# Kernel tuning notes

Hardware: AMD Instinct MI355X
Metric: run time of the kernel (lower is better)

The kernel has to match this reference:

```python
import jax, jax.numpy as jnp
import numpy as np

TEMPERATURE = 0.01  # clamped min is 0.01, so constant temp stays 0.01
MASK_VAL = -10000.0


def setup_inputs() -> dict:
    key = jax.random.key(0)
    k1, k2 = jax.random.split(key)
    B, C, D = 512, 16, 128
    ts_features = jax.random.normal(k1, (B, C, D), dtype=jnp.float32)
    note_features = jax.random.normal(k2, (B, C, D), dtype=jnp.float32)
    return {"ts_features": ts_features, "note_features": note_features}


def reference(ts_features, note_features):
    B, C, D = ts_features.shape
    N = B * C
    ts = ts_features.reshape(N, D)
    nt = note_features.reshape(N, D)

    # sim[i, j] = <ts_i, nt_j>
    sim = jnp.einsum('id,jd->ij', ts, nt)

    # block-diagonal mask: within each CxC block, off-diagonal -> -10000, diagonal kept
    idx = jnp.arange(N)
    blk = idx // C
    same_block = blk[:, None] == blk[None, :]
    is_diag = idx[:, None] == idx[None, :]
    sim_new = jnp.where(same_block & ~is_diag, jnp.asarray(MASK_VAL, sim.dtype), sim)

    logits = sim_new / TEMPERATURE
    # cross entropy with labels = arange(N), both directions
    lsm_r = jax.nn.log_softmax(logits, axis=-1)
    lsm_c = jax.nn.log_softmax(logits.T, axis=-1)
    diag_ids = (idx, idx)
    ce_r = -jnp.mean(lsm_r[diag_ids])
    ce_c = -jnp.mean(lsm_c[diag_ids])
    total_loss = (ce_r + ce_c) / 2

    # nan/inf -> 0 as in the original
    total_loss = jnp.where(jnp.isnan(total_loss) | jnp.isinf(total_loss),
                           jnp.asarray(0.0, total_loss.dtype), total_loss)
    return total_loss
```

## Files before the change

### kernel.cpp

```cpp
#include <hip/hip_runtime.h>
#include <stdint.h>

#define NROWS 8192
#define DDIM  128
#define PPART 8
#define BROWS 256
#define NITER 16
#define LOG2E_X100 144.26950408889634f
#define LN2F       0.6931471805599453f

typedef __bf16 bf16x8 __attribute__((ext_vector_type(8)));
typedef float  f32x4  __attribute__((ext_vector_type(4)));

__device__ __forceinline__ unsigned short f2bf_rne(float f) {
    union { float f; uint32_t u; } v; v.f = f;
    uint32_t r = (v.u + 0x7FFFu + ((v.u >> 16) & 1u)) >> 16;
    return (unsigned short)r;
}

__device__ __forceinline__ void async16(const unsigned short* g, unsigned char* l) {
    __builtin_amdgcn_global_load_lds(
        (const __attribute__((address_space(1))) unsigned int*)g,
        (__attribute__((address_space(3))) unsigned int*)l, 16, 0, 0);
}

__global__ void convert_kernel(const float* __restrict__ ts, const float* __restrict__ nt,
                               unsigned short* __restrict__ ts_bf,
                               unsigned short* __restrict__ nt_bf,
                               float* __restrict__ acc, int* __restrict__ ticket) {
    const int nvec = (NROWS * DDIM) / 4;
    int tid = blockIdx.x * blockDim.x + threadIdx.x;
    bool isNT = tid >= nvec;
    int i = isNT ? (tid - nvec) : tid;
    const float4 v = ((const float4*)(isNT ? nt : ts))[i];
    float sc = isNT ? 1.0f : LOG2E_X100;
    ushort4 o;
    o.x = f2bf_rne(v.x * sc); o.y = f2bf_rne(v.y * sc);
    o.z = f2bf_rne(v.z * sc); o.w = f2bf_rne(v.w * sc);
    ((ushort4*)(isNT ? nt_bf : ts_bf))[i] = o;
    if (tid == 0) { *acc = 0.0f; *ticket = 0; }
}

__device__ __forceinline__ void dma_stage(const unsigned short* g, unsigned char* l,
                                          int lane, int wv) {
#pragma unroll
    for (int k = 0; k < 2; ++k) {
        int u = wv * 2 + k;
        int r = u * 4 + (lane >> 4);
        int ch = (lane & 15) ^ (r & 7);
        async16(g + r * 128 + ch * 8, l + u * 1024);
    }
}

__global__ __launch_bounds__(512, 4) void rowstats_kernel(
        const unsigned short* __restrict__ ts_bf,
        const unsigned short* __restrict__ nt_bf,
        float* __restrict__ pm, float* __restrict__ ps, float* __restrict__ pd) {
    __shared__ unsigned char smem[2 * 16384];

    const int lane = threadIdx.x & 63;
    const int wv   = threadIdx.x >> 6;
    const int c    = lane & 15;
    const int quad = lane >> 4;
    const int bx   = blockIdx.x;
    const int part = blockIdx.y;
    const int dir  = blockIdx.z;
    const int rows0 = bx * BROWS + wv * 32;

    const unsigned short* A = dir ? nt_bf : ts_bf;
    const unsigned short* B = dir ? ts_bf : nt_bf;

    bf16x8 a[2][4];
#pragma unroll
    for (int s = 0; s < 2; ++s) {
        const unsigned short* abase = A + (rows0 + s * 16 + c) * DDIM + quad * 8;
#pragma unroll
        for (int kc = 0; kc < 4; ++kc)
            a[s][kc] = *(const bf16x8*)(abase + kc * 32);
    }

    float m[2][4], ss[2][4], dg[2][4];
#pragma unroll
    for (int s = 0; s < 2; ++s)
#pragma unroll
        for (int r = 0; r < 4; ++r) { m[s][r] = -INFINITY; ss[s][r] = 0.0f; dg[s][r] = 0.0f; }

    const bool havePart = (part == (bx >> 2));
    const int  t_d = (bx & 3) * 4 + (wv >> 1);
    const int  l0  = (wv & 1) * 2;

    const unsigned short* bwalk = B + part * (NROWS / PPART) * DDIM;

    dma_stage(bwalk, smem, lane, wv);
    __syncthreads();

    for (int t = 0; t < NITER; ++t) {
        if (t + 1 < NITER)
            dma_stage(bwalk + (t + 1) * 64 * DDIM, smem + ((t + 1) & 1) * 16384, lane, wv);

        const unsigned char* buf = smem + (t & 1) * 16384;

        f32x4 acc[4][2];
#pragma unroll
        for (int l = 0; l < 4; ++l)
#pragma unroll
            for (int s = 0; s < 2; ++s) acc[l][s] = (f32x4){0.f, 0.f, 0.f, 0.f};

#pragma unroll
        for (int kc = 0; kc < 4; ++kc) {
            const int sw = ((kc * 4 + quad) ^ (c & 7)) * 16;
            const unsigned char* p = buf + c * 256 + sw;
            bf16x8 b0 = *(const bf16x8*)(p);
            bf16x8 b1 = *(const bf16x8*)(p + 4096);
            bf16x8 b2 = *(const bf16x8*)(p + 8192);
            bf16x8 b3 = *(const bf16x8*)(p + 12288);
            acc[0][0] = __builtin_amdgcn_mfma_f32_16x16x32_bf16(a[0][kc], b0, acc[0][0], 0, 0, 0);
            acc[0][1] = __builtin_amdgcn_mfma_f32_16x16x32_bf16(a[1][kc], b0, acc[0][1], 0, 0, 0);
            acc[1][0] = __builtin_amdgcn_mfma_f32_16x16x32_bf16(a[0][kc], b1, acc[1][0], 0, 0, 0);
            acc[1][1] = __builtin_amdgcn_mfma_f32_16x16x32_bf16(a[1][kc], b1, acc[1][1], 0, 0, 0);
            acc[2][0] = __builtin_amdgcn_mfma_f32_16x16x32_bf16(a[0][kc], b2, acc[2][0], 0, 0, 0);
            acc[2][1] = __builtin_amdgcn_mfma_f32_16x16x32_bf16(a[1][kc], b2, acc[2][1], 0, 0, 0);
            acc[3][0] = __builtin_amdgcn_mfma_f32_16x16x32_bf16(a[0][kc], b3, acc[3][0], 0, 0, 0);
            acc[3][1] = __builtin_amdgcn_mfma_f32_16x16x32_bf16(a[1][kc], b3, acc[3][1], 0, 0, 0);
        }

        const bool pd_ = havePart && (t == t_d);
#pragma unroll
        for (int s = 0; s < 2; ++s) {
#pragma unroll
            for (int r = 0; r < 4; ++r) {
                float x0 = acc[0][s][r], x1 = acc[1][s][r];
                float x2 = acc[2][s][r], x3 = acc[3][s][r];
                if (pd_) {
                    const int dslot = l0 + s;
                    bool onDiag = (c == quad * 4 + r);
                    float xv = dslot == 0 ? x0 : dslot == 1 ? x1 : dslot == 2 ? x2 : x3;
                    if (onDiag) dg[s][r] += xv;
                    float rep = onDiag ? xv : -1.0e30f;
                    if (dslot == 0) x0 = rep; else if (dslot == 1) x1 = rep;
                    else if (dslot == 2) x2 = rep; else x3 = rep;
                }
                float mn = fmaxf(fmaxf(fmaxf(x0, x1), fmaxf(x2, x3)), m[s][r]);
                float e  = __builtin_amdgcn_exp2f(m[s][r] - mn);
                float es = (__builtin_amdgcn_exp2f(x0 - mn) + __builtin_amdgcn_exp2f(x1 - mn))
                         + (__builtin_amdgcn_exp2f(x2 - mn) + __builtin_amdgcn_exp2f(x3 - mn));
                ss[s][r] = fmaf(ss[s][r], e, es);
                m[s][r] = mn;
            }
        }
        __syncthreads();
    }

#pragma unroll
    for (int s = 0; s < 2; ++s) {
#pragma unroll
        for (int r = 0; r < 4; ++r) {
            float mm = m[s][r];
#pragma unroll
            for (int off = 1; off < 16; off <<= 1)
                mm = fmaxf(mm, __shfl_xor(mm, off, 64));
            float sv = ss[s][r] * __builtin_amdgcn_exp2f(m[s][r] - mm);
            float dd = dg[s][r];
#pragma unroll
            for (int off = 1; off < 16; off <<= 1) {
                sv += __shfl_xor(sv, off, 64);
                dd += __shfl_xor(dd, off, 64);
            }
            if (c == 0) {
                int row = rows0 + s * 16 + quad * 4 + r;
                int idx = (dir * NROWS + row) * PPART + part;
                pm[idx] = mm; ps[idx] = sv; pd[idx] = dd;
            }
        }
    }
}

__global__ void merge_kernel(const float* __restrict__ pm, const float* __restrict__ ps,
                             const float* __restrict__ pd, float* __restrict__ acc,
                             int* __restrict__ ticket, float* __restrict__ out) {
    int tid = blockIdx.x * blockDim.x + threadIdx.x;
    const float* pmr = pm + tid * PPART;
    const float* psr = ps + tid * PPART;
    const float* pdr = pd + tid * PPART;
    float mt = -INFINITY;
#pragma unroll
    for (int p = 0; p < PPART; ++p) mt = fmaxf(mt, pmr[p]);
    float st = 0.0f, dt = 0.0f;
#pragma unroll
    for (int p = 0; p < PPART; ++p) {
        st += psr[p] * __builtin_amdgcn_exp2f(pmr[p] - mt);
        dt += pdr[p];
    }
    float lsm = dt - mt - __builtin_amdgcn_logf(st);

    float v = lsm;
#pragma unroll
    for (int off = 32; off; off >>= 1) v += __shfl_down(v, off, 64);
    __shared__ float wsum[4];
    if ((threadIdx.x & 63) == 0) wsum[threadIdx.x >> 6] = v;
    __syncthreads();
    if (threadIdx.x == 0) {
        atomicAdd(acc, wsum[0] + wsum[1] + wsum[2] + wsum[3]);
        __threadfence();
        int old = atomicAdd(ticket, 1);
        if (old == (int)gridDim.x - 1) {
            __threadfence();
            float tot = atomicAdd(acc, 0.0f);
            float t = -(tot * LN2F) / (2.0f * NROWS);
            if (!isfinite(t)) t = 0.0f;
            out[0] = t;
        }
    }
}

extern "C" void kernel_launch(void* const* d_in, const int* in_sizes, int n_in,
                              void* d_out, int out_size, void* d_ws, size_t ws_size,
                              hipStream_t stream) {
    const float* ts = (const float*)d_in[0];
    const float* nt = (const float*)d_in[1];
    float* out = (float*)d_out;

    unsigned short* ts_bf = (unsigned short*)d_ws;
    unsigned short* nt_bf = ts_bf + NROWS * DDIM;
    float* pm = (float*)(nt_bf + NROWS * DDIM);
    float* ps = pm + 2 * NROWS * PPART;
    float* pd = ps + 2 * NROWS * PPART;
    float* acc = pd + 2 * NROWS * PPART;
    int* ticket = (int*)(acc + 1);

    convert_kernel<<<2048, 256, 0, stream>>>(ts, nt, ts_bf, nt_bf, acc, ticket);
    rowstats_kernel<<<dim3(NROWS / BROWS, PPART, 2), 512, 0, stream>>>(ts_bf, nt_bf, pm, ps, pd);
    merge_kernel<<<(2 * NROWS) / 256, 256, 0, stream>>>(pm, ps, pd, acc, ticket, out);
}
```

Baseline: 110.0 us.

## Drop LDS staging for direct B loads and fuse merge into rowstats kernel

The rowstats kernel no longer stages B tiles into LDS with async global_load_lds double buffering. Each wave now loads B fragments straight from global memory into registers, which removes the per-iteration __syncthreads. The separate merge kernel is folded into rowstats: per-(dir, block-row) counters pick the last of the partition blocks to finish, and that block merges the partial stats and adds its sum to the global accumulator. This removes one kernel launch and the extra pass over the partials. In exchange, B reuse across the 8 waves now depends on the L1/L2 caches, and there is extra atomic and fence traffic at the end of each block.

```diff
diff --git a/kernel.cpp b/kernel.cpp
--- a/kernel.cpp
+++ b/kernel.cpp
@@ -18,16 +18,10 @@
     return (unsigned short)r;
 }
 
-__device__ __forceinline__ void async16(const unsigned short* g, unsigned char* l) {
-    __builtin_amdgcn_global_load_lds(
-        (const __attribute__((address_space(1))) unsigned int*)g,
-        (__attribute__((address_space(3))) unsigned int*)l, 16, 0, 0);
-}
-
 __global__ void convert_kernel(const float* __restrict__ ts, const float* __restrict__ nt,
                                unsigned short* __restrict__ ts_bf,
                                unsigned short* __restrict__ nt_bf,
-                               float* __restrict__ acc, int* __restrict__ ticket) {
+                               float* __restrict__ acc, int* __restrict__ ctrl) {
     const int nvec = (NROWS * DDIM) / 4;
     int tid = blockIdx.x * blockDim.x + threadIdx.x;
     bool isNT = tid >= nvec;
@@ -38,26 +32,15 @@
     o.x = f2bf_rne(v.x * sc); o.y = f2bf_rne(v.y * sc);
     o.z = f2bf_rne(v.z * sc); o.w = f2bf_rne(v.w * sc);
     ((ushort4*)(isNT ? nt_bf : ts_bf))[i] = o;
-    if (tid == 0) { *acc = 0.0f; *ticket = 0; }
-}
-
-__device__ __forceinline__ void dma_stage(const unsigned short* g, unsigned char* l,
-                                          int lane, int wv) {
-#pragma unroll
-    for (int k = 0; k < 2; ++k) {
-        int u = wv * 2 + k;
-        int r = u * 4 + (lane >> 4);
-        int ch = (lane & 15) ^ (r & 7);
-        async16(g + r * 128 + ch * 8, l + u * 1024);
-    }
+    if (tid < 65) ctrl[tid] = 0;
+    if (tid == 65) *acc = 0.0f;
 }
 
 __global__ __launch_bounds__(512, 4) void rowstats_kernel(
         const unsigned short* __restrict__ ts_bf,
         const unsigned short* __restrict__ nt_bf,
-        float* __restrict__ pm, float* __restrict__ ps, float* __restrict__ pd) {
-    __shared__ unsigned char smem[2 * 16384];
-
+        float* __restrict__ pm, float* __restrict__ ps, float* __restrict__ pd,
+        float* __restrict__ acc, int* __restrict__ ctrl, float* __restrict__ out) {
     const int lane = threadIdx.x & 63;
     const int wv   = threadIdx.x >> 6;
     const int c    = lane & 15;
@@ -89,48 +72,43 @@
     const int  t_d = (bx & 3) * 4 + (wv >> 1);
     const int  l0  = (wv & 1) * 2;
 
-    const unsigned short* bwalk = B + part * (NROWS / PPART) * DDIM;
-
-    dma_stage(bwalk, smem, lane, wv);
-    __syncthreads();
+    const unsigned short* bp[4];
+#pragma unroll
+    for (int l = 0; l < 4; ++l)
+        bp[l] = B + (part * (NROWS / PPART) + l * 16 + c) * DDIM + quad * 8;
 
     for (int t = 0; t < NITER; ++t) {
-        if (t + 1 < NITER)
-            dma_stage(bwalk + (t + 1) * 64 * DDIM, smem + ((t + 1) & 1) * 16384, lane, wv);
-
-        const unsigned char* buf = smem + (t & 1) * 16384;
-
-        f32x4 acc[4][2];
+        f32x4 av[4][2];
 #pragma unroll
         for (int l = 0; l < 4; ++l)
 #pragma unroll
-            for (int s = 0; s < 2; ++s) acc[l][s] = (f32x4){0.f, 0.f, 0.f, 0.f};
+            for (int s = 0; s < 2; ++s) av[l][s] = (f32x4){0.f, 0.f, 0.f, 0.f};
 
 #pragma unroll
         for (int kc = 0; kc < 4; ++kc) {
-            const int sw = ((kc * 4 + quad) ^ (c & 7)) * 16;
-            const unsigned char* p = buf + c * 256 + sw;
-            bf16x8 b0 = *(const bf16x8*)(p);
-            bf16x8 b1 = *(const bf16x8*)(p + 4096);
-            bf16x8 b2 = *(const bf16x8*)(p + 8192);
-            bf16x8 b3 = *(const bf16x8*)(p + 12288);
-            acc[0][0] = __builtin_amdgcn_mfma_f32_16x16x32_bf16(a[0][kc], b0, acc[0][0], 0, 0, 0);
-            acc[0][1] = __builtin_amdgcn_mfma_f32_16x16x32_bf16(a[1][kc], b0, acc[0][1], 0, 0, 0);
-            acc[1][0] = __builtin_amdgcn_mfma_f32_16x16x32_bf16(a[0][kc], b1, acc[1][0], 0, 0, 0);
-            acc[1][1] = __builtin_amdgcn_mfma_f32_16x16x32_bf16(a[1][kc], b1, acc[1][1], 0, 0, 0);
-            acc[2][0] = __builtin_amdgcn_mfma_f32_16x16x32_bf16(a[0][kc], b2, acc[2][0], 0, 0, 0);
-            acc[2][1] = __builtin_amdgcn_mfma_f32_16x16x32_bf16(a[1][kc], b2, acc[2][1], 0, 0, 0);
-            acc[3][0] = __builtin_amdgcn_mfma_f32_16x16x32_bf16(a[0][kc], b3, acc[3][0], 0, 0, 0);
-            acc[3][1] = __builtin_amdgcn_mfma_f32_16x16x32_bf16(a[1][kc], b3, acc[3][1], 0, 0, 0);
-        }
+            bf16x8 b0 = *(const bf16x8*)(bp[0] + kc * 32);
+            bf16x8 b1 = *(const bf16x8*)(bp[1] + kc * 32);
+            bf16x8 b2 = *(const bf16x8*)(bp[2] + kc * 32);
+            bf16x8 b3 = *(const bf16x8*)(bp[3] + kc * 32);
+            av[0][0] = __builtin_amdgcn_mfma_f32_16x16x32_bf16(a[0][kc], b0, av[0][0], 0, 0, 0);
+            av[0][1] = __builtin_amdgcn_mfma_f32_16x16x32_bf16(a[1][kc], b0, av[0][1], 0, 0, 0);
+            av[1][0] = __builtin_amdgcn_mfma_f32_16x16x32_bf16(a[0][kc], b1, av[1][0], 0, 0, 0);
+            av[1][1] = __builtin_amdgcn_mfma_f32_16x16x32_bf16(a[1][kc], b1, av[1][1], 0, 0, 0);
+            av[2][0] = __builtin_amdgcn_mfma_f32_16x16x32_bf16(a[0][kc], b2, av[2][0], 0, 0, 0);
+            av[2][1] = __builtin_amdgcn_mfma_f32_16x16x32_bf16(a[1][kc], b2, av[2][1], 0, 0, 0);
+            av[3][0] = __builtin_amdgcn_mfma_f32_16x16x32_bf16(a[0][kc], b3, av[3][0], 0, 0, 0);
+            av[3][1] = __builtin_amdgcn_mfma_f32_16x16x32_bf16(a[1][kc], b3, av[3][1], 0, 0, 0);
+        }
+#pragma unroll
+        for (int l = 0; l < 4; ++l) bp[l] += 64 * DDIM;
 
         const bool pd_ = havePart && (t == t_d);
 #pragma unroll
         for (int s = 0; s < 2; ++s) {
 #pragma unroll
             for (int r = 0; r < 4; ++r) {
-                float x0 = acc[0][s][r], x1 = acc[1][s][r];
-                float x2 = acc[2][s][r], x3 = acc[3][s][r];
+                float x0 = av[0][s][r], x1 = av[1][s][r];
+                float x2 = av[2][s][r], x3 = av[3][s][r];
                 if (pd_) {
                     const int dslot = l0 + s;
                     bool onDiag = (c == quad * 4 + r);
@@ -148,7 +126,6 @@
                 m[s][r] = mn;
             }
         }
-        __syncthreads();
     }
 
 #pragma unroll
@@ -173,42 +150,51 @@
             }
         }
     }
-}
-
-__global__ void merge_kernel(const float* __restrict__ pm, const float* __restrict__ ps,
-                             const float* __restrict__ pd, float* __restrict__ acc,
-                             int* __restrict__ ticket, float* __restrict__ out) {
-    int tid = blockIdx.x * blockDim.x + threadIdx.x;
-    const float* pmr = pm + tid * PPART;
-    const float* psr = ps + tid * PPART;
-    const float* pdr = pd + tid * PPART;
-    float mt = -INFINITY;
-#pragma unroll
-    for (int p = 0; p < PPART; ++p) mt = fmaxf(mt, pmr[p]);
-    float st = 0.0f, dt = 0.0f;
-#pragma unroll
-    for (int p = 0; p < PPART; ++p) {
-        st += psr[p] * __builtin_amdgcn_exp2f(pmr[p] - mt);
-        dt += pdr[p];
-    }
-    float lsm = dt - mt - __builtin_amdgcn_logf(st);
-
-    float v = lsm;
-#pragma unroll
-    for (int off = 32; off; off >>= 1) v += __shfl_down(v, off, 64);
-    __shared__ float wsum[4];
-    if ((threadIdx.x & 63) == 0) wsum[threadIdx.x >> 6] = v;
+
+    __threadfence();
+    __shared__ int sflag;
+    __shared__ float wsum[8];
+    if (threadIdx.x == 0) {
+        int old = atomicAdd(&ctrl[dir * 32 + bx], 1);
+        sflag = (old == PPART - 1) ? 1 : 0;
+    }
     __syncthreads();
-    if (threadIdx.x == 0) {
-        atomicAdd(acc, wsum[0] + wsum[1] + wsum[2] + wsum[3]);
+    if (sflag) {
         __threadfence();
-        int old = atomicAdd(ticket, 1);
-        if (old == (int)gridDim.x - 1) {
+        float lsm = 0.0f;
+        if (threadIdx.x < BROWS) {
+            int row = bx * BROWS + threadIdx.x;
+            int idx = (dir * NROWS + row) * PPART;
+            float mt = -INFINITY;
+#pragma unroll
+            for (int p = 0; p < PPART; ++p) mt = fmaxf(mt, pm[idx + p]);
+            float st = 0.0f, dt = 0.0f;
+#pragma unroll
+            for (int p = 0; p < PPART; ++p) {
+                st += ps[idx + p] * __builtin_amdgcn_exp2f(pm[idx + p] - mt);
+                dt += pd[idx + p];
+            }
+            lsm = dt - mt - __builtin_amdgcn_logf(st);
+        }
+        float v = lsm;
+#pragma unroll
+        for (int off = 32; off; off >>= 1) v += __shfl_down(v, off, 64);
+        if (lane == 0) wsum[wv] = v;
+        __syncthreads();
+        if (threadIdx.x == 0) {
+            float bsum = 0.0f;
+#pragma unroll
+            for (int w = 0; w < 8; ++w) bsum += wsum[w];
+            atomicAdd(acc, bsum);
             __threadfence();
-            float tot = atomicAdd(acc, 0.0f);
-            float t = -(tot * LN2F) / (2.0f * NROWS);
-            if (!isfinite(t)) t = 0.0f;
-            out[0] = t;
+            int old = atomicAdd(&ctrl[64], 1);
+            if (old == 63) {
+                __threadfence();
+                float tot = atomicAdd(acc, 0.0f);
+                float t = -(tot * LN2F) / (2.0f * NROWS);
+                if (!isfinite(t)) t = 0.0f;
+                out[0] = t;
+            }
         }
     }
 }
@@ -226,9 +212,9 @@
     float* ps = pm + 2 * NROWS * PPART;
     float* pd = ps + 2 * NROWS * PPART;
     float* acc = pd + 2 * NROWS * PPART;
-    int* ticket = (int*)(acc + 1);
-
-    convert_kernel<<<2048, 256, 0, stream>>>(ts, nt, ts_bf, nt_bf, acc, ticket);
-    rowstats_kernel<<<dim3(NROWS / BROWS, PPART, 2), 512, 0, stream>>>(ts_bf, nt_bf, pm, ps, pd);
-    merge_kernel<<<(2 * NROWS) / 256, 256, 0, stream>>>(pm, ps, pd, acc, ticket, out);
-}
+    int* ctrl = (int*)(acc + 1);
+
+    convert_kernel<<<2048, 256, 0, stream>>>(ts, nt, ts_bf, nt_bf, acc, ctrl);
+    rowstats_kernel<<<dim3(NROWS / BROWS, PPART, 2), 512, 0, stream>>>(
+        ts_bf, nt_bf, pm, ps, pd, acc, ctrl, out);
+}
```

New measurement: 310.3 us. +182.1%, slower.

## Pre-swizzle bf16 operands into MFMA fragment order during conversion

Applied to the files above, without the earlier changes.

The conversion kernel now writes the bf16 copies in a tiled layout that matches the MFMA 16x16x32 fragment order, with each thread handling 8 elements and emitting one 16-byte store. The main kernel can then load A fragments and stage B tiles with fully contiguous per-lane 16-byte accesses, dropping the XOR swizzle address math. The aim is fewer address computations, better-coalesced global and LDS accesses, and fewer conversion threads. The trade-off is that the conversion kernel's stores become scattered, and correctness depends on the new layout matching the fragment indexing exactly.

```diff
diff --git a/kernel.cpp b/kernel.cpp
--- a/kernel.cpp
+++ b/kernel.cpp
@@ -11,6 +11,8 @@
 
 typedef __bf16 bf16x8 __attribute__((ext_vector_type(8)));
 typedef float  f32x4  __attribute__((ext_vector_type(4)));
+typedef unsigned short u16x8 __attribute__((ext_vector_type(8)));
+
 
 __device__ __forceinline__ unsigned short f2bf_rne(float f) {
     union { float f; uint32_t u; } v; v.f = f;
@@ -28,16 +30,23 @@
                                unsigned short* __restrict__ ts_bf,
                                unsigned short* __restrict__ nt_bf,
                                float* __restrict__ acc, int* __restrict__ ticket) {
-    const int nvec = (NROWS * DDIM) / 4;
+    const int nchunk = (NROWS * DDIM) / 8;
     int tid = blockIdx.x * blockDim.x + threadIdx.x;
-    bool isNT = tid >= nvec;
-    int i = isNT ? (tid - nvec) : tid;
-    const float4 v = ((const float4*)(isNT ? nt : ts))[i];
+    bool isNT = tid >= nchunk;
+    int i = isNT ? (tid - nchunk) : tid;
+    const float4* src = (const float4*)(isNT ? nt : ts) + i * 2;
+    float4 v0 = src[0], v1 = src[1];
     float sc = isNT ? 1.0f : LOG2E_X100;
-    ushort4 o;
-    o.x = f2bf_rne(v.x * sc); o.y = f2bf_rne(v.y * sc);
-    o.z = f2bf_rne(v.z * sc); o.w = f2bf_rne(v.w * sc);
-    ((ushort4*)(isNT ? nt_bf : ts_bf))[i] = o;
+    u16x8 o;
+    o[0] = f2bf_rne(v0.x * sc); o[1] = f2bf_rne(v0.y * sc);
+    o[2] = f2bf_rne(v0.z * sc); o[3] = f2bf_rne(v0.w * sc);
+    o[4] = f2bf_rne(v1.x * sc); o[5] = f2bf_rne(v1.y * sc);
+    o[6] = f2bf_rne(v1.z * sc); o[7] = f2bf_rne(v1.w * sc);
+    int row = i >> 4, chunk = i & 15;
+    int g = row >> 4, c = row & 15;
+    int kc = chunk >> 2, quad = chunk & 3;
+    int off16 = (g * 4 + kc) * 64 + quad * 16 + c;
+    ((u16x8*)(isNT ? nt_bf : ts_bf))[off16] = o;
     if (tid == 0) { *acc = 0.0f; *ticket = 0; }
 }
 
@@ -46,9 +55,7 @@
 #pragma unroll
     for (int k = 0; k < 2; ++k) {
         int u = wv * 2 + k;
-        int r = u * 4 + (lane >> 4);
-        int ch = (lane & 15) ^ (r & 7);
-        async16(g + r * 128 + ch * 8, l + u * 1024);
+        async16(g + u * 512 + lane * 8, l + u * 1024);
     }
 }
 
@@ -70,14 +77,13 @@
     const unsigned short* A = dir ? nt_bf : ts_bf;
     const unsigned short* B = dir ? ts_bf : nt_bf;
 
+    const int G0 = bx * 16 + wv * 2;
     bf16x8 a[2][4];
 #pragma unroll
-    for (int s = 0; s < 2; ++s) {
-        const unsigned short* abase = A + (rows0 + s * 16 + c) * DDIM + quad * 8;
+    for (int s = 0; s < 2; ++s)
 #pragma unroll
         for (int kc = 0; kc < 4; ++kc)
-            a[s][kc] = *(const bf16x8*)(abase + kc * 32);
-    }
+            a[s][kc] = *(const bf16x8*)(A + ((G0 + s) * 4 + kc) * 512 + lane * 8);
 
     float m[2][4], ss[2][4], dg[2][4];
 #pragma unroll
@@ -89,39 +95,37 @@
     const int  t_d = (bx & 3) * 4 + (wv >> 1);
     const int  l0  = (wv & 1) * 2;
 
-    const unsigned short* bwalk = B + part * (NROWS / PPART) * DDIM;
+    const unsigned short* bwalk = B + part * 64 * 2048;
 
     dma_stage(bwalk, smem, lane, wv);
     __syncthreads();
 
     for (int t = 0; t < NITER; ++t) {
         if (t + 1 < NITER)
-            dma_stage(bwalk + (t + 1) * 64 * DDIM, smem + ((t + 1) & 1) * 16384, lane, wv);
-
-        const unsigned char* buf = smem + (t & 1) * 16384;
-
-        f32x4 acc[4][2];
+            dma_stage(bwalk + (t + 1) * 8192, smem + ((t + 1) & 1) * 16384, lane, wv);
+
+        const unsigned char* buf = smem + (t & 1) * 16384 + lane * 16;
+
+        f32x4 av[4][2];
 #pragma unroll
         for (int l = 0; l < 4; ++l)
 #pragma unroll
-            for (int s = 0; s < 2; ++s) acc[l][s] = (f32x4){0.f, 0.f, 0.f, 0.f};
+            for (int s = 0; s < 2; ++s) av[l][s] = (f32x4){0.f, 0.f, 0.f, 0.f};
 
 #pragma unroll
         for (int kc = 0; kc < 4; ++kc) {
-            const int sw = ((kc * 4 + quad) ^ (c & 7)) * 16;
-            const unsigned char* p = buf + c * 256 + sw;
-            bf16x8 b0 = *(const bf16x8*)(p);
-            bf16x8 b1 = *(const bf16x8*)(p + 4096);
-            bf16x8 b2 = *(const bf16x8*)(p + 8192);
-            bf16x8 b3 = *(const bf16x8*)(p + 12288);
-            acc[0][0] = __builtin_amdgcn_mfma_f32_16x16x32_bf16(a[0][kc], b0, acc[0][0], 0, 0, 0);
-            acc[0][1] = __builtin_amdgcn_mfma_f32_16x16x32_bf16(a[1][kc], b0, acc[0][1], 0, 0, 0);
-            acc[1][0] = __builtin_amdgcn_mfma_f32_16x16x32_bf16(a[0][kc], b1, acc[1][0], 0, 0, 0);
-            acc[1][1] = __builtin_amdgcn_mfma_f32_16x16x32_bf16(a[1][kc], b1, acc[1][1], 0, 0, 0);
-            acc[2][0] = __builtin_amdgcn_mfma_f32_16x16x32_bf16(a[0][kc], b2, acc[2][0], 0, 0, 0);
-            acc[2][1] = __builtin_amdgcn_mfma_f32_16x16x32_bf16(a[1][kc], b2, acc[2][1], 0, 0, 0);
-            acc[3][0] = __builtin_amdgcn_mfma_f32_16x16x32_bf16(a[0][kc], b3, acc[3][0], 0, 0, 0);
-            acc[3][1] = __builtin_amdgcn_mfma_f32_16x16x32_bf16(a[1][kc], b3, acc[3][1], 0, 0, 0);
+            bf16x8 b0 = *(const bf16x8*)(buf + kc * 1024);
+            bf16x8 b1 = *(const bf16x8*)(buf + kc * 1024 + 4096);
+            bf16x8 b2 = *(const bf16x8*)(buf + kc * 1024 + 8192);
+            bf16x8 b3 = *(const bf16x8*)(buf + kc * 1024 + 12288);
+            av[0][0] = __builtin_amdgcn_mfma_f32_16x16x32_bf16(a[0][kc], b0, av[0][0], 0, 0, 0);
+            av[0][1] = __builtin_amdgcn_mfma_f32_16x16x32_bf16(a[1][kc], b0, av[0][1], 0, 0, 0);
+            av[1][0] = __builtin_amdgcn_mfma_f32_16x16x32_bf16(a[0][kc], b1, av[1][0], 0, 0, 0);
+            av[1][1] = __builtin_amdgcn_mfma_f32_16x16x32_bf16(a[1][kc], b1, av[1][1], 0, 0, 0);
+            av[2][0] = __builtin_amdgcn_mfma_f32_16x16x32_bf16(a[0][kc], b2, av[2][0], 0, 0, 0);
+            av[2][1] = __builtin_amdgcn_mfma_f32_16x16x32_bf16(a[1][kc], b2, av[2][1], 0, 0, 0);
+            av[3][0] = __builtin_amdgcn_mfma_f32_16x16x32_bf16(a[0][kc], b3, av[3][0], 0, 0, 0);
+            av[3][1] = __builtin_amdgcn_mfma_f32_16x16x32_bf16(a[1][kc], b3, av[3][1], 0, 0, 0);
         }
 
         const bool pd_ = havePart && (t == t_d);
@@ -129,8 +133,8 @@
         for (int s = 0; s < 2; ++s) {
 #pragma unroll
             for (int r = 0; r < 4; ++r) {
-                float x0 = acc[0][s][r], x1 = acc[1][s][r];
-                float x2 = acc[2][s][r], x3 = acc[3][s][r];
+                float x0 = av[0][s][r], x1 = av[1][s][r];
+                float x2 = av[2][s][r], x3 = av[3][s][r];
                 if (pd_) {
                     const int dslot = l0 + s;
                     bool onDiag = (c == quad * 4 + r);
@@ -228,7 +232,7 @@
     float* acc = pd + 2 * NROWS * PPART;
     int* ticket = (int*)(acc + 1);
 
-    convert_kernel<<<2048, 256, 0, stream>>>(ts, nt, ts_bf, nt_bf, acc, ticket);
+    convert_kernel<<<1024, 256, 0, stream>>>(ts, nt, ts_bf, nt_bf, acc, ticket);
     rowstats_kernel<<<dim3(NROWS / BROWS, PPART, 2), 512, 0, stream>>>(ts_bf, nt_bf, pm, ps, pd);
     merge_kernel<<<(2 * NROWS) / 256, 256, 0, stream>>>(pm, ps, pd, acc, ticket, out);
 }
```

After: 107.4 us. 1.02x faster.
